# Performance work log

Measured on AMD Instinct MI355X. Metric: run time of the kernel, lower is better.

The kernel has to match this reference:

```python
import jax, jax.numpy as jnp
import numpy as np

B, P, ENC = 128, 196, 2048   # batch, num_pixels (14x14), encoder_dim
A, H, E, V = 512, 512, 512, 10000  # attention_dim, hidden, embed, vocab
T = 20  # max decode length (lengths max = T+1)


def setup_inputs() -> dict:
    key = jax.random.key(0)
    ks = jax.random.split(key, 24)
    def rn(k, shape, scale=0.05):
        return jax.random.normal(k, shape, jnp.float32) * scale
    encoder_out = jax.random.normal(ks[0], (B, P, ENC), jnp.float32)
    captions = jax.random.randint(ks[1], (B, T + 1), 0, V)
    # lengths sorted descending (packed-sequence convention), max forced to T+1
    lengths = jnp.sort(jax.random.randint(ks[2], (B,), 2, T + 2))[::-1]
    lengths = lengths.at[0].set(T + 1)
    return {
        "encoder_out": encoder_out,
        "captions": captions,
        "lengths": lengths,
        "W_enc_att": rn(ks[3], (A, ENC)), "b_enc_att": jnp.zeros((A,), jnp.float32),
        "W_dec_att": rn(ks[4], (A, H)),   "b_dec_att": jnp.zeros((A,), jnp.float32),
        "w_full_att": rn(ks[5], (1, A)),  "b_full_att": jnp.zeros((1,), jnp.float32),
        "emb_table": rn(ks[6], (V, E)),
        "W_ih": rn(ks[7], (4 * H, E + ENC)), "b_ih": jnp.zeros((4 * H,), jnp.float32),
        "W_hh": rn(ks[8], (4 * H, H)),       "b_hh": jnp.zeros((4 * H,), jnp.float32),
        "W_init_h": rn(ks[9], (H, ENC)),  "b_init_h": jnp.zeros((H,), jnp.float32),
        "W_init_c": rn(ks[10], (H, ENC)), "b_init_c": jnp.zeros((H,), jnp.float32),
        "W_fbeta": rn(ks[11], (ENC, H)),  "b_fbeta": jnp.zeros((ENC,), jnp.float32),
        "W_fc": rn(ks[12], (V, H)),       "b_fc": jnp.zeros((V,), jnp.float32),
    }


def reference(encoder_out, captions, lengths,
              W_enc_att, b_enc_att, W_dec_att, b_dec_att, w_full_att, b_full_att,
              emb_table, W_ih, b_ih, W_hh, b_hh,
              W_init_h, b_init_h, W_init_c, b_init_c,
              W_fbeta, b_fbeta, W_fc, b_fc):
    # Precompute encoder side of Bahdanau attention once (loop-invariant)
    att1 = jnp.einsum('bpe,ae->bpa', encoder_out, W_enc_att) + b_enc_att  # [B,P,A]
    emb = emb_table[captions]                                            # [B,T+1,E]
    mean_enc = encoder_out.mean(axis=1)                                  # [B,ENC]
    h0 = mean_enc @ W_init_h.T + b_init_h
    c0 = mean_enc @ W_init_c.T + b_init_c
    dec_len = lengths - 1
    # mask[t, b] = True while sample b still decodes at step t (== torch's b < batch_size_t for sorted lengths)
    mask = (jnp.arange(T)[:, None] < dec_len[None, :]).astype(encoder_out.dtype)  # [T,B]
    xs = (jnp.swapaxes(emb[:, :T, :], 0, 1), mask)  # ([T,B,E], [T,B])

    def step(carry, x):
        h, c = carry
        emb_t, m = x  # [B,E], [B]
        # Bahdanau attention
        att2 = h @ W_dec_att.T + b_dec_att                               # [B,A]
        e = jnp.einsum('bpa,a->bp', jax.nn.relu(att1 + att2[:, None, :]),
                       w_full_att[0]) + b_full_att[0]                    # [B,P]
        alpha = jax.nn.softmax(e, axis=1)
        context = jnp.einsum('bp,bpe->be', alpha, encoder_out)           # [B,ENC]
        gate = jax.nn.sigmoid(h @ W_fbeta.T + b_fbeta)
        context = gate * context
        # LSTMCell (PyTorch gate order: i, f, g, o); dropout is identity in eval mode
        x_in = jnp.concatenate([emb_t, context], axis=1)                 # [B,E+ENC]
        gates = x_in @ W_ih.T + b_ih + h @ W_hh.T + b_hh                 # [B,4H]
        i, f, g, o = jnp.split(gates, 4, axis=1)
        c_new = jax.nn.sigmoid(f) * c + jax.nn.sigmoid(i) * jnp.tanh(g)
        h_new = jax.nn.sigmoid(o) * jnp.tanh(c_new)
        pred = (h_new @ W_fc.T + b_fc) * m[:, None]                      # zeros past length
        mb = m[:, None]
        h = mb * h_new + (1.0 - mb) * h   # freeze state for finished rows
        c = mb * c_new + (1.0 - mb) * c
        return (h, c), pred

    (_, _), preds = jax.lax.scan(step, (h0, c0), xs)
    return jnp.swapaxes(preds, 0, 1)  # [B,T,V]
```

## Files before the change

### kernel.cpp

```cpp
#include <hip/hip_runtime.h>
#include <hip/hip_bf16.h>
#include <math.h>

#define B_   128
#define P_   196
#define ENC_ 2048
#define A_   512
#define H_   512
#define E_   512
#define V_   10000
#define T_   20
#define NDF_ 2560
#define XK_  3072
#define GK_  2560

typedef __attribute__((ext_vector_type(8))) short bf16x8;
typedef __attribute__((ext_vector_type(4))) short bf16x4;
typedef __attribute__((ext_vector_type(2))) short bf16x2;
typedef __attribute__((ext_vector_type(4))) float f32x4;

__device__ __forceinline__ float sigmoidf_(float x) { return 1.0f / (1.0f + expf(-x)); }

__device__ __forceinline__ short f2bf(float f) {
    unsigned u = __float_as_uint(f);
    u += 0x7fffu + ((u >> 16) & 1u);
    return (short)(u >> 16);
}
__device__ __forceinline__ float bf2f(short s) {
    return __uint_as_float(((unsigned)(unsigned short)s) << 16);
}
__device__ __forceinline__ void gload_lds16(const void* g, void* l) {
    __builtin_amdgcn_global_load_lds(
        (const __attribute__((address_space(1))) void*)g,
        (__attribute__((address_space(3))) void*)l, 16, 0, 0);
}

#define BM 128
#define BN 64
#define BK 64

#define COMPUTE64(ASP, BSP, CUR)                                               \
    _Pragma("unroll")                                                          \
    for (int kk = 0; kk < BK; kk += 32) {                                      \
        const int kb = (kk >> 3) + (lane >> 4);                                \
        bf16x8 av[4], bv[2];                                                   \
        _Pragma("unroll")                                                      \
        for (int i = 0; i < 4; i++) {                                          \
            int rr = wr * 64 + i * 16 + (lane & 15);                           \
            av[i] = *(const bf16x8*)&(ASP)[(CUR) * (BM * BK) + rr * BK         \
                    + ((kb ^ (rr & 7)) << 3)];                                 \
        }                                                                      \
        _Pragma("unroll")                                                      \
        for (int j = 0; j < 2; j++) {                                          \
            int cc = wc * 32 + j * 16 + (lane & 15);                           \
            bv[j] = *(const bf16x8*)&(BSP)[(CUR) * (BN * BK) + cc * BK         \
                    + ((kb ^ (cc & 7)) << 3)];                                 \
        }                                                                      \
        _Pragma("unroll")                                                      \
        for (int i = 0; i < 4; i++)                                            \
            _Pragma("unroll")                                                  \
            for (int j = 0; j < 2; j++)                                        \
                acc[i][j] = __builtin_amdgcn_mfma_f32_16x16x32_bf16(           \
                    av[i], bv[j], acc[i][j], 0, 0, 0);                         \
    }

__global__ __launch_bounds__(256) void gemm_bf(
    const short* __restrict__ A, const short* __restrict__ Bw,
    float* __restrict__ Cf, short* __restrict__ Cb,
    const float* __restrict__ bias,
    int N, int K, int lda, int ldb, int ldc,
    int mtiles, int ntiles, int mode,
    const int* __restrict__ lengths)
{
    __shared__ __attribute__((aligned(16))) short As[2][BM * BK];
    __shared__ __attribute__((aligned(16))) short Bs[2][BN * BK];
    int pm, pn;
    if (mtiles == 1) { pm = 0; pn = blockIdx.x; }
    else {
        int xcd = blockIdx.x & 7, s = blockIdx.x >> 3;
        pn = s % ntiles;
        pm = (s / ntiles) * 8 + xcd;
        if (pm >= mtiles) return;
    }
    const int bm = pm * BM, bn = pn * BN;
    const int tid = threadIdx.x, w = tid >> 6, lane = tid & 63;
    const int wr = w >> 1, wc = w & 1;
    const int lr8 = lane >> 3, lk = lane & 7;

    f32x4 zero4 = {0.f, 0.f, 0.f, 0.f};
    f32x4 acc[4][2];
    #pragma unroll
    for (int i = 0; i < 4; i++)
        #pragma unroll
        for (int j = 0; j < 2; j++) acc[i][j] = zero4;

#define STAGE(buf, k0) {                                                        \
    _Pragma("unroll")                                                           \
    for (int i = 0; i < 4; i++) {                                               \
        int row0 = w * 32 + i * 8; int row = row0 + lr8;                        \
        gload_lds16(A + (size_t)(bm + row) * lda + (k0)                         \
                    + ((lk ^ (row & 7)) << 3), &As[buf][row0 * BK]);            \
    }                                                                           \
    _Pragma("unroll")                                                           \
    for (int i = 0; i < 2; i++) {                                               \
        int row0 = w * 16 + i * 8; int row = row0 + lr8;                        \
        int gn = bn + row; if (gn > N - 1) gn = N - 1;                          \
        gload_lds16(Bw + (size_t)gn * ldb + (k0)                                \
                    + ((lk ^ (row & 7)) << 3), &Bs[buf][row0 * BK]);            \
    } }

    STAGE(0, 0);
    __syncthreads();
    int cur = 0;
    for (int k0 = 0; k0 < K; k0 += BK) {
        if (k0 + BK < K) STAGE(cur ^ 1, k0 + BK);
        COMPUTE64(&As[0][0], &Bs[0][0], cur);
        __syncthreads();
        cur ^= 1;
    }
#undef STAGE

    const int lr = lane >> 4, lc = lane & 15;
    #pragma unroll
    for (int i = 0; i < 4; i++) {
        #pragma unroll
        for (int r = 0; r < 4; r++) {
            int row = bm + wr * 64 + i * 16 + lr * 4 + r;
            #pragma unroll
            for (int j = 0; j < 2; j++) {
                int col = bn + wc * 32 + j * 16 + lc;
                if (col >= N) continue;
                float v = acc[i][j][r] + bias[col];
                if (mode == 1) {
                    int tt = row >> 7, bb = row & 127;
                    float rs = (tt < lengths[bb] - 1) ? 1.0f : 0.0f;
                    Cf[(size_t)bb * T_ * V_ + (size_t)tt * V_ + col] = v * rs;
                } else if (mode == 2) {
                    if (col < H_) Cb[(size_t)row * H_ + col] = f2bf(v);
                    else          Cf[(size_t)row * H_ + (col - H_)] = v;
                } else if (Cb) {
                    Cb[(size_t)row * ldc + col] = f2bf(v);
                } else {
                    Cf[(size_t)row * ldc + col] = v;
                }
            }
        }
    }
}

__global__ __launch_bounds__(256) void att1_gemm(
    const float* __restrict__ A, const short* __restrict__ Bw,
    short* __restrict__ Cb, const float* __restrict__ bias)
{
    __shared__ __attribute__((aligned(16))) short As[2][BM * BK];
    __shared__ __attribute__((aligned(16))) short Bs[2][BN * BK];
    int xcd = blockIdx.x & 7, s = blockIdx.x >> 3;
    int pn = s % 8;
    int pm = (s / 8) * 8 + xcd;
    if (pm >= 196) return;
    const int bm = pm * BM, bn = pn * BN;
    const int tid = threadIdx.x, w = tid >> 6, lane = tid & 63;
    const int wr = w >> 1, wc = w & 1;
    const int lr8 = lane >> 3, lk = lane & 7;

    f32x4 zero4 = {0.f, 0.f, 0.f, 0.f};
    f32x4 acc[4][2];
    #pragma unroll
    for (int i = 0; i < 4; i++)
        #pragma unroll
        for (int j = 0; j < 2; j++) acc[i][j] = zero4;

    float4 ra[4][2];
#define LOADA(k0) {                                                             \
    _Pragma("unroll")                                                           \
    for (int i = 0; i < 4; i++) {                                               \
        int row = w * 32 + i * 8 + lr8;                                         \
        const float* ga = A + (size_t)(bm + row) * ENC_ + (k0)                  \
                          + ((lk ^ (row & 7)) << 3);                            \
        ra[i][0] = *(const float4*)ga;                                          \
        ra[i][1] = *(const float4*)(ga + 4);                                    \
    } }
#define WRITEA(buf) {                                                           \
    _Pragma("unroll")                                                           \
    for (int i = 0; i < 4; i++) {                                               \
        int row = w * 32 + i * 8 + lr8;                                         \
        bf16x8 v;                                                               \
        v[0] = f2bf(ra[i][0].x); v[1] = f2bf(ra[i][0].y);                       \
        v[2] = f2bf(ra[i][0].z); v[3] = f2bf(ra[i][0].w);                       \
        v[4] = f2bf(ra[i][1].x); v[5] = f2bf(ra[i][1].y);                       \
        v[6] = f2bf(ra[i][1].z); v[7] = f2bf(ra[i][1].w);                       \
        *(bf16x8*)&As[buf][row * BK + (lk << 3)] = v;                           \
    } }
#define BSTAGE(buf, k0) {                                                       \
    _Pragma("unroll")                                                           \
    for (int i = 0; i < 2; i++) {                                               \
        int row0 = w * 16 + i * 8; int row = row0 + lr8;                        \
        gload_lds16(Bw + (size_t)(bn + row) * ENC_ + (k0)                       \
                    + ((lk ^ (row & 7)) << 3), &Bs[buf][row0 * BK]);            \
    } }

    LOADA(0);
    BSTAGE(0, 0);
    WRITEA(0);
    __syncthreads();
    int cur = 0;
    for (int k0 = 0; k0 < ENC_; k0 += BK) {
        if (k0 + BK < ENC_) { LOADA(k0 + BK); BSTAGE(cur ^ 1, k0 + BK); }
        COMPUTE64(&As[0][0], &Bs[0][0], cur);
        if (k0 + BK < ENC_) WRITEA(cur ^ 1);
        __syncthreads();
        cur ^= 1;
    }
#undef LOADA
#undef WRITEA
#undef BSTAGE

    const int lr = lane >> 4, lc = lane & 15;
    #pragma unroll
    for (int i = 0; i < 4; i++)
        #pragma unroll
        for (int r = 0; r < 4; r++) {
            int row = bm + wr * 64 + i * 16 + lr * 4 + r;
            #pragma unroll
            for (int j = 0; j < 2; j++) {
                int col = bn + wc * 32 + j * 16 + lc;
                Cb[(size_t)row * A_ + col] = f2bf(acc[i][j][r] + bias[col]);
            }
        }
}

__global__ __launch_bounds__(512) void esmctx_kernel(
    const short* __restrict__ att1_bf, const float* __restrict__ attf,
    const float* __restrict__ wfull, const short* __restrict__ enc_bf,
    short* __restrict__ ctxbuf, const int* __restrict__ lengths, int t)
{
    __shared__ float es[P_];
    __shared__ float red[256];
    __shared__ float al[P_];
    __shared__ float sm, ss;
    const int b = blockIdx.y, half = blockIdx.x;
    if (t >= lengths[b] - 1) return;
    const int tid = threadIdx.x, wv = tid >> 6, lane = tid & 63;

    float a2v[8], wv8[8];
    const float* a2 = attf + (size_t)b * NDF_;
    #pragma unroll
    for (int i = 0; i < 8; i++) {
        a2v[i] = a2[lane * 8 + i];
        wv8[i] = wfull[lane * 8 + i];
    }
    for (int row = wv; row < P_; row += 8) {
        bf16x8 a1 = *(const bf16x8*)(att1_bf + ((size_t)b * P_ + row) * A_ + lane * 8);
        float s = 0.0f;
        #pragma unroll
        for (int i = 0; i < 8; i++) {
            float v = bf2f(a1[i]) + a2v[i];
            s += fmaxf(v, 0.0f) * wv8[i];
        }
        #pragma unroll
        for (int off = 32; off > 0; off >>= 1) s += __shfl_down(s, off, 64);
        if (lane == 0) es[row] = s;
    }
    __syncthreads();
    float v = (tid < P_) ? es[tid] : -1e30f;
    if (tid < 256) red[tid] = v;
    __syncthreads();
    for (int rs = 128; rs > 0; rs >>= 1) {
        if (tid < rs) red[tid] = fmaxf(red[tid], red[tid + rs]);
        __syncthreads();
    }
    if (tid == 0) sm = red[0];
    __syncthreads();
    float ex = (tid < P_) ? expf(v - sm) : 0.0f;
    if (tid < 256) red[tid] = ex;
    __syncthreads();
    for (int rs = 128; rs > 0; rs >>= 1) {
        if (tid < rs) red[tid] += red[tid + rs];
        __syncthreads();
    }
    if (tid == 0) ss = red[0];
    __syncthreads();
    if (tid < P_) al[tid] = ex / ss;
    __syncthreads();

    const int c0 = half * 1024 + tid * 2;
    const short* eb = enc_bf + (size_t)b * P_ * ENC_ + c0;
    float s0 = 0, s1 = 0;
    for (int p = 0; p < P_; p++) {
        bf16x2 ev = *(const bf16x2*)(eb + (size_t)p * ENC_);
        float a = al[p];
        s0 += a * bf2f(ev[0]); s1 += a * bf2f(ev[1]);
    }
    const float* fb = attf + (size_t)b * NDF_ + A_;
    bf16x2 o;
    o[0] = f2bf(sigmoidf_(fb[c0 + 0]) * s0);
    o[1] = f2bf(sigmoidf_(fb[c0 + 1]) * s1);
    *(bf16x2*)(ctxbuf + (size_t)b * ENC_ + c0) = o;
}

__global__ __launch_bounds__(256) void gates_lstm(
    const short* __restrict__ ctxbuf, const short* __restrict__ hcur,
    short* __restrict__ hnxt,
    const short* __restrict__ Wcat, const float* __restrict__ gpre,
    float* __restrict__ cbuf, short* __restrict__ hn_t,
    const int* __restrict__ lengths, int t)
{
    __shared__ __attribute__((aligned(16))) char smem[49152];
    short* As0 = (short*)smem;
    short* Bs0 = (short*)(smem + 32768);
    const int bn = blockIdx.x * BN;
    const int tid = threadIdx.x, w = tid >> 6, lane = tid & 63;
    const int wr = w >> 1, wc = w & 1;
    const int lr8 = lane >> 3, lk = lane & 7;

    f32x4 zero4 = {0.f, 0.f, 0.f, 0.f};
    f32x4 acc[4][2];
    #pragma unroll
    for (int i = 0; i < 4; i++)
        #pragma unroll
        for (int j = 0; j < 2; j++) acc[i][j] = zero4;

#define STAGE_G(buf, k0) {                                                      \
    const short* Ap; int Al, kk0;                                               \
    if ((k0) < ENC_) { Ap = ctxbuf; Al = ENC_; kk0 = (k0); }                    \
    else             { Ap = hcur;   Al = H_;   kk0 = (k0) - ENC_; }             \
    _Pragma("unroll")                                                           \
    for (int i = 0; i < 4; i++) {                                               \
        int row0 = w * 32 + i * 8; int row = row0 + lr8;                        \
        gload_lds16(Ap + (size_t)row * Al + kk0 + ((lk ^ (row & 7)) << 3),      \
                    &As0[(buf) * (BM * BK) + row0 * BK]);                       \
    }                                                                           \
    _Pragma("unroll")                                                           \
    for (int i = 0; i < 2; i++) {                                               \
        int row0 = w * 16 + i * 8; int row = row0 + lr8;                        \
        gload_lds16(Wcat + (size_t)(bn + row) * XK_ + E_ + (k0)                 \
                    + ((lk ^ (row & 7)) << 3),                                  \
                    &Bs0[(buf) * (BN * BK) + row0 * BK]);                       \
    } }

    STAGE_G(0, 0);
    __syncthreads();
    int cur = 0;
    for (int k0 = 0; k0 < GK_; k0 += BK) {
        if (k0 + BK < GK_) STAGE_G(cur ^ 1, k0 + BK);
        COMPUTE64(As0, Bs0, cur);
        __syncthreads();
        cur ^= 1;
    }
#undef STAGE_G

    float* gl = (float*)smem;
    const int lr = lane >> 4, lc = lane & 15;
    #pragma unroll
    for (int i = 0; i < 4; i++)
        #pragma unroll
        for (int r = 0; r < 4; r++) {
            int row = wr * 64 + i * 16 + lr * 4 + r;
            #pragma unroll
            for (int j = 0; j < 2; j++) {
                int col = wc * 32 + j * 16 + lc;
                gl[row * 68 + col] = acc[i][j][r] + gpre[(size_t)row * (4 * H_) + bn + col];
            }
        }
    __syncthreads();
    #pragma unroll
    for (int q = 0; q < 8; q++) {
        int id  = tid * 8 + q;
        int row = id >> 4;
        int j   = id & 15;
        int jg  = (bn >> 2) + j;
        float i_ = sigmoidf_(gl[row * 68 + 4 * j + 0]);
        float f_ = sigmoidf_(gl[row * 68 + 4 * j + 1]);
        float g_ = tanhf    (gl[row * 68 + 4 * j + 2]);
        float o_ = sigmoidf_(gl[row * 68 + 4 * j + 3]);
        float cn = f_ * cbuf[row * H_ + jg] + i_ * g_;
        float hv = o_ * tanhf(cn);
        hn_t[row * H_ + jg] = f2bf(hv);
        bool m = t < lengths[row] - 1;
        if (m) cbuf[row * H_ + jg] = cn;
        hnxt[row * H_ + jg] = m ? f2bf(hv) : hcur[row * H_ + jg];
    }
}

__global__ __launch_bounds__(256) void castenc_mean(const float* __restrict__ enc,
                                                    short* __restrict__ enc_bf,
                                                    short* __restrict__ meanE_bf)
{
    const int b = blockIdx.y;
    const int c0 = blockIdx.x * 1024 + threadIdx.x * 4;
    const float* src = enc + (size_t)b * P_ * ENC_ + c0;
    short* dst = enc_bf + (size_t)b * P_ * ENC_ + c0;
    float s0 = 0, s1 = 0, s2 = 0, s3 = 0;
    for (int p = 0; p < P_; p++) {
        float4 f = *(const float4*)(src + (size_t)p * ENC_);
        bf16x4 v;
        v[0] = f2bf(f.x); v[1] = f2bf(f.y); v[2] = f2bf(f.z); v[3] = f2bf(f.w);
        *(bf16x4*)(dst + (size_t)p * ENC_) = v;
        s0 += f.x; s1 += f.y; s2 += f.z; s3 += f.w;
    }
    const float inv = 1.0f / (float)P_;
    bf16x4 m;
    m[0] = f2bf(s0 * inv); m[1] = f2bf(s1 * inv);
    m[2] = f2bf(s2 * inv); m[3] = f2bf(s3 * inv);
    *(bf16x4*)(meanE_bf + (size_t)b * ENC_ + c0) = m;
}

#define PB0 1024
#define PB1 (PB0 + 2048)
#define PB2 (PB1 + 5000)
#define PB3 (PB2 + 1280)
#define PB4 (PB3 + 6144)
#define PB5 (PB4 + 1280)
#define PB6 (PB5 + 3)
#define PB7 (PB6 + 2)
#define PB8 (PB7 + 1)

__device__ __forceinline__ void cast4(const float* __restrict__ in,
                                      short* __restrict__ out, int i4) {
    float4 f = *(const float4*)(in + i4);
    bf16x4 v;
    v[0] = f2bf(f.x); v[1] = f2bf(f.y); v[2] = f2bf(f.z); v[3] = f2bf(f.w);
    *(bf16x4*)(out + i4) = v;
}
__device__ __forceinline__ void cast4p(const float* __restrict__ src,
                                       short* __restrict__ out, int i4) {
    float4 f = *(const float4*)src;
    bf16x4 v;
    v[0] = f2bf(f.x); v[1] = f2bf(f.y); v[2] = f2bf(f.z); v[3] = f2bf(f.w);
    *(bf16x4*)(out + i4) = v;
}

__global__ __launch_bounds__(256) void prep_kernel(
    const float* __restrict__ W_enc,    const float* __restrict__ W_init_h,
    const float* __restrict__ W_init_c, const float* __restrict__ W_fc,
    const float* __restrict__ W_dec,    const float* __restrict__ W_fbeta,
    const float* __restrict__ W_ih,     const float* __restrict__ W_hh,
    const int*   __restrict__ captions, const float* __restrict__ emb_tab,
    const float* __restrict__ b_dec,    const float* __restrict__ b_fbeta,
    const float* __restrict__ b_ih,     const float* __restrict__ b_hh,
    const float* __restrict__ b_init_h, const float* __restrict__ b_init_c,
    short* __restrict__ Wenc_bf,  short* __restrict__ Winit_bf,
    short* __restrict__ Wfc_bf,   short* __restrict__ Wdf_bf,
    short* __restrict__ Wcat_bf,  short* __restrict__ emb_all,
    float* __restrict__ bdf,      float* __restrict__ bcat,
    float* __restrict__ binit)
{
    const int blk = blockIdx.x, tid = threadIdx.x;
    if (blk < PB0) {
        cast4(W_enc, Wenc_bf, blk * 1024 + tid * 4);
    } else if (blk < PB1) {
        int i4 = (blk - PB0) * 1024 + tid * 4;
        int n = i4 >> 11, k = i4 & 2047;
        const float* src = (n < H_) ? W_init_h + (size_t)n * ENC_ + k
                                    : W_init_c + (size_t)(n - H_) * ENC_ + k;
        cast4p(src, Winit_bf, i4);
    } else if (blk < PB2) {
        cast4(W_fc, Wfc_bf, (blk - PB1) * 1024 + tid * 4);
    } else if (blk < PB3) {
        int i4 = (blk - PB2) * 1024 + tid * 4;
        int n = i4 >> 9, k = i4 & 511;
        const float* src = (n < A_) ? W_dec + (size_t)n * H_ + k
                                    : W_fbeta + (size_t)(n - A_) * H_ + k;
        cast4p(src, Wdf_bf, i4);
    } else if (blk < PB4) {
        int i4 = (blk - PB3) * 1024 + tid * 4;
        int n = i4 / XK_, k = i4 - n * XK_;
        int srow = (n & 3) * H_ + (n >> 2);
        const float* src = (k < E_ + ENC_) ? W_ih + (size_t)srow * (E_ + ENC_) + k
                                           : W_hh + (size_t)srow * H_ + (k - (E_ + ENC_));
        cast4p(src, Wcat_bf, i4);
    } else if (blk < PB5) {
        int i4 = (blk - PB4) * 1024 + tid * 4;
        int col = i4 & 511;
        int bt  = i4 >> 9;
        int b   = bt & 127;
        int tt  = bt >> 7;
        int tok = captions[b * (T_ + 1) + tt];
        cast4p(emb_tab + (size_t)tok * E_ + col, emb_all, i4);
    } else if (blk < PB6) {
        int j = (blk - PB5) * 1024 + tid * 4;
        #pragma unroll
        for (int q = 0; q < 4; q++, j++)
            if (j < NDF_) bdf[j] = (j < A_) ? b_dec[j] : b_fbeta[j - A_];
    } else if (blk < PB7) {
        int j = (blk - PB6) * 1024 + tid * 4;
        #pragma unroll
        for (int q = 0; q < 4; q++, j++) {
            int srow = (j & 3) * H_ + (j >> 2);
            bcat[j] = b_ih[srow] + b_hh[srow];
        }
    } else {
        int j = tid * 4;
        #pragma unroll
        for (int q = 0; q < 4; q++, j++)
            binit[j] = (j < H_) ? b_init_h[j] : b_init_c[j - H_];
    }
}

extern "C" void kernel_launch(void* const* d_in, const int* in_sizes, int n_in,
                              void* d_out, int out_size, void* d_ws, size_t ws_size,
                              hipStream_t stream)
{
    const float* enc      = (const float*)d_in[0];
    const int*   captions = (const int*)  d_in[1];
    const int*   lengths  = (const int*)  d_in[2];
    const float* W_enc    = (const float*)d_in[3];
    const float* b_enc    = (const float*)d_in[4];
    const float* W_dec    = (const float*)d_in[5];
    const float* b_dec    = (const float*)d_in[6];
    const float* w_full   = (const float*)d_in[7];
    const float* emb_tab  = (const float*)d_in[9];
    const float* W_ih     = (const float*)d_in[10];
    const float* b_ih     = (const float*)d_in[11];
    const float* W_hh     = (const float*)d_in[12];
    const float* b_hh     = (const float*)d_in[13];
    const float* W_init_h = (const float*)d_in[14];
    const float* b_init_h = (const float*)d_in[15];
    const float* W_init_c = (const float*)d_in[16];
    const float* b_init_c = (const float*)d_in[17];
    const float* W_fbeta  = (const float*)d_in[18];
    const float* b_fbeta  = (const float*)d_in[19];
    const float* W_fc     = (const float*)d_in[20];
    const float* b_fc     = (const float*)d_in[21];
    float* out = (float*)d_out;

    char* ws = (char*)d_ws;
    size_t off = 0;
    auto alloc = [&](size_t bytes) { void* p = ws + off; off += (bytes + 255) & ~(size_t)255; return p; };
    short* enc_bf    = (short*)alloc((size_t)B_ * P_ * ENC_ * 2);
    short* att1_bf   = (short*)alloc((size_t)B_ * P_ * A_ * 2);
    short* Wenc_bf   = (short*)alloc((size_t)A_ * ENC_ * 2);
    short* Winit_bf  = (short*)alloc((size_t)2 * H_ * ENC_ * 2);
    short* Wdf_bf    = (short*)alloc((size_t)NDF_ * H_ * 2);
    short* Wcat_bf   = (short*)alloc((size_t)4 * H_ * XK_ * 2);
    short* Wfc_bf    = (short*)alloc((size_t)V_ * H_ * 2);
    float* bdf       = (float*)alloc(NDF_ * 4);
    float* bcat      = (float*)alloc(4 * H_ * 4);
    float* binit     = (float*)alloc(2 * H_ * 4);
    short* meanE_bf  = (short*)alloc((size_t)B_ * ENC_ * 2);
    float* cbuf      = (float*)alloc((size_t)B_ * H_ * 4);
    short* hbufs     = (short*)alloc((size_t)2 * B_ * H_ * 2);
    short* emb_all   = (short*)alloc((size_t)T_ * B_ * E_ * 2);
    short* hn_all    = (short*)alloc((size_t)T_ * B_ * H_ * 2);
    float* attf      = (float*)alloc((size_t)B_ * NDF_ * 4);
    short* ctxbuf    = (short*)alloc((size_t)B_ * ENC_ * 2);
    float* gates_pre = (float*)alloc((size_t)T_ * B_ * 4 * H_ * 4);
    (void)ws_size;

    prep_kernel<<<PB8, 256, 0, stream>>>(
        W_enc, W_init_h, W_init_c, W_fc, W_dec, W_fbeta, W_ih, W_hh,
        captions, emb_tab, b_dec, b_fbeta, b_ih, b_hh, b_init_h, b_init_c,
        Wenc_bf, Winit_bf, Wfc_bf, Wdf_bf, Wcat_bf, emb_all, bdf, bcat, binit);

    att1_gemm<<<8 * 8 * ((196 + 7) / 8), 256, 0, stream>>>(
        enc, Wenc_bf, att1_bf, b_enc);
    castenc_mean<<<dim3(2, B_), 256, 0, stream>>>(enc, enc_bf, meanE_bf);
    gemm_bf<<<8 * 32 * (((T_ * B_) / BM + 7) / 8), 256, 0, stream>>>(
        emb_all, Wcat_bf, gates_pre, nullptr, bcat,
        4 * H_, E_, E_, XK_, 4 * H_, (T_ * B_) / BM, 32, 0, nullptr);
    gemm_bf<<<(2 * H_) / BN, 256, 0, stream>>>(
        meanE_bf, Winit_bf, cbuf, hbufs, binit,
        2 * H_, ENC_, ENC_, ENC_, 0, 1, (2 * H_) / BN, 2, nullptr);

    for (int t = 0; t < T_; t++) {
        short* hcur = hbufs + (size_t)(t & 1) * B_ * H_;
        short* hnxt = hbufs + (size_t)((t & 1) ^ 1) * B_ * H_;
        gemm_bf<<<NDF_ / BN, 256, 0, stream>>>(
            hcur, Wdf_bf, attf, nullptr, bdf,
            NDF_, H_, H_, H_, NDF_, 1, NDF_ / BN, 0, nullptr);
        esmctx_kernel<<<dim3(2, B_), 512, 0, stream>>>(
            att1_bf, attf, w_full, enc_bf, ctxbuf, lengths, t);
        gates_lstm<<<(4 * H_) / BN, 256, 0, stream>>>(
            ctxbuf, hcur, hnxt, Wcat_bf, gates_pre + (size_t)t * B_ * 4 * H_,
            cbuf, hn_all + (size_t)t * B_ * H_, lengths, t);
    }
    gemm_bf<<<8 * 157 * (((T_ * B_) / BM + 7) / 8), 256, 0, stream>>>(
        hn_all, Wfc_bf, out, nullptr, b_fc,
        V_, H_, H_, H_, 0, (T_ * B_) / BM, 157, 1, lengths);
}
```

Baseline: 1.883 ms.

## Fuse decode loop into persistent cooperative kernel with grid barriers

The 20-step decode loop, previously three kernel launches per step (attention projection GEMM, energy/softmax/context, gates+LSTM), becomes a single cooperative persistent kernel of 256 blocks that synchronise through an atomic-counter grid barrier between phases. This is meant to remove about 60 launch gaps and their tail effects. The att1 GEMM also now reads the already bf16-cast encoder through the generic gemm_bf path, dropping the dedicated fp32-input kernel. The cost is three spin barriers per step and idle blocks in the GEMM phases; if the cooperative launch fails, the old launch loop runs instead.

```diff
diff --git a/kernel.cpp b/kernel.cpp
--- a/kernel.cpp
+++ b/kernel.cpp
@@ -13,6 +13,7 @@
 #define NDF_ 2560
 #define XK_  3072
 #define GK_  2560
+#define NBLK_ 256
 
 typedef __attribute__((ext_vector_type(8))) short bf16x8;
 typedef __attribute__((ext_vector_type(4))) short bf16x4;
@@ -148,85 +149,238 @@
     }
 }
 
-__global__ __launch_bounds__(256) void att1_gemm(
-    const float* __restrict__ A, const short* __restrict__ Bw,
-    short* __restrict__ Cb, const float* __restrict__ bias)
+__device__ __forceinline__ void gbar(unsigned* cnt, unsigned target) {
+    __syncthreads();
+    if (threadIdx.x == 0) {
+        __hip_atomic_fetch_add(cnt, 1u, __ATOMIC_RELEASE, __HIP_MEMORY_SCOPE_AGENT);
+        while (__hip_atomic_fetch_add(cnt, 0u, __ATOMIC_RELAXED, __HIP_MEMORY_SCOPE_AGENT) < target)
+            __builtin_amdgcn_s_sleep(8);
+        (void)__hip_atomic_load(cnt, __ATOMIC_ACQUIRE, __HIP_MEMORY_SCOPE_AGENT);
+    }
+    __syncthreads();
+}
+
+__global__ __launch_bounds__(512) void loop_kernel(
+    const short* __restrict__ att1_bf, const short* __restrict__ enc_bf,
+    const short* __restrict__ Wdf, const float* __restrict__ bdf,
+    const float* __restrict__ wfull, const short* __restrict__ Wcat,
+    const float* __restrict__ gates_pre,
+    short* __restrict__ hbufs, float* __restrict__ cbuf,
+    short* __restrict__ hn_all, float* __restrict__ attf,
+    short* __restrict__ ctxbuf, const int* __restrict__ lengths,
+    unsigned* __restrict__ cnt)
 {
-    __shared__ __attribute__((aligned(16))) short As[2][BM * BK];
-    __shared__ __attribute__((aligned(16))) short Bs[2][BN * BK];
-    int xcd = blockIdx.x & 7, s = blockIdx.x >> 3;
-    int pn = s % 8;
-    int pm = (s / 8) * 8 + xcd;
-    if (pm >= 196) return;
-    const int bm = pm * BM, bn = pn * BN;
-    const int tid = threadIdx.x, w = tid >> 6, lane = tid & 63;
-    const int wr = w >> 1, wc = w & 1;
+    __shared__ __attribute__((aligned(16))) char smem[49152];
+    const int blk = blockIdx.x, tid = threadIdx.x;
+    const int lane = tid & 63;
+    const bool act = tid < 256;
+    const int w4 = (tid >> 6) & 3;
+    const int wr = w4 >> 1, wc = w4 & 1;
     const int lr8 = lane >> 3, lk = lane & 7;
-
-    f32x4 zero4 = {0.f, 0.f, 0.f, 0.f};
-    f32x4 acc[4][2];
-    #pragma unroll
-    for (int i = 0; i < 4; i++)
-        #pragma unroll
-        for (int j = 0; j < 2; j++) acc[i][j] = zero4;
-
-    float4 ra[4][2];
-#define LOADA(k0) {                                                             \
+    const int lr = lane >> 4, lc = lane & 15;
+    unsigned bar = 0;
+
+#define STAGE_A(buf, k0) if (act) {                                             \
     _Pragma("unroll")                                                           \
     for (int i = 0; i < 4; i++) {                                               \
-        int row = w * 32 + i * 8 + lr8;                                         \
-        const float* ga = A + (size_t)(bm + row) * ENC_ + (k0)                  \
-                          + ((lk ^ (row & 7)) << 3);                            \
-        ra[i][0] = *(const float4*)ga;                                          \
-        ra[i][1] = *(const float4*)(ga + 4);                                    \
+        int row0 = w4 * 32 + i * 8; int row = row0 + lr8;                       \
+        gload_lds16(hcur + (size_t)row * H_ + (k0) + ((lk ^ (row & 7)) << 3),   \
+                    &As0[(buf) * (BM * BK) + row0 * BK]);                       \
+    }                                                                           \
+    _Pragma("unroll")                                                           \
+    for (int i = 0; i < 2; i++) {                                               \
+        int row0 = w4 * 16 + i * 8; int row = row0 + lr8;                       \
+        gload_lds16(Wdf + (size_t)(bn + row) * H_ + (k0)                        \
+                    + ((lk ^ (row & 7)) << 3),                                  \
+                    &Bs0[(buf) * (BN * BK) + row0 * BK]);                       \
     } }
-#define WRITEA(buf) {                                                           \
+
+#define STAGE_C(buf, k0) if (act) {                                             \
+    const short* Ap; int Al, kk0;                                               \
+    if ((k0) < ENC_) { Ap = ctxbuf; Al = ENC_; kk0 = (k0); }                    \
+    else             { Ap = hcur;   Al = H_;   kk0 = (k0) - ENC_; }             \
     _Pragma("unroll")                                                           \
     for (int i = 0; i < 4; i++) {                                               \
-        int row = w * 32 + i * 8 + lr8;                                         \
-        bf16x8 v;                                                               \
-        v[0] = f2bf(ra[i][0].x); v[1] = f2bf(ra[i][0].y);                       \
-        v[2] = f2bf(ra[i][0].z); v[3] = f2bf(ra[i][0].w);                       \
-        v[4] = f2bf(ra[i][1].x); v[5] = f2bf(ra[i][1].y);                       \
-        v[6] = f2bf(ra[i][1].z); v[7] = f2bf(ra[i][1].w);                       \
-        *(bf16x8*)&As[buf][row * BK + (lk << 3)] = v;                           \
-    } }
-#define BSTAGE(buf, k0) {                                                       \
+        int row0 = w4 * 32 + i * 8; int row = row0 + lr8;                       \
+        gload_lds16(Ap + (size_t)row * Al + kk0 + ((lk ^ (row & 7)) << 3),      \
+                    &As0[(buf) * (BM * BK) + row0 * BK]);                       \
+    }                                                                           \
     _Pragma("unroll")                                                           \
     for (int i = 0; i < 2; i++) {                                               \
-        int row0 = w * 16 + i * 8; int row = row0 + lr8;                        \
-        gload_lds16(Bw + (size_t)(bn + row) * ENC_ + (k0)                       \
-                    + ((lk ^ (row & 7)) << 3), &Bs[buf][row0 * BK]);            \
+        int row0 = w4 * 16 + i * 8; int row = row0 + lr8;                       \
+        gload_lds16(Wcat + (size_t)(bn + row) * XK_ + E_ + (k0)                 \
+                    + ((lk ^ (row & 7)) << 3),                                  \
+                    &Bs0[(buf) * (BN * BK) + row0 * BK]);                       \
     } }
 
-    LOADA(0);
-    BSTAGE(0, 0);
-    WRITEA(0);
-    __syncthreads();
-    int cur = 0;
-    for (int k0 = 0; k0 < ENC_; k0 += BK) {
-        if (k0 + BK < ENC_) { LOADA(k0 + BK); BSTAGE(cur ^ 1, k0 + BK); }
-        COMPUTE64(&As[0][0], &Bs[0][0], cur);
-        if (k0 + BK < ENC_) WRITEA(cur ^ 1);
-        __syncthreads();
-        cur ^= 1;
-    }
-#undef LOADA
-#undef WRITEA
-#undef BSTAGE
-
-    const int lr = lane >> 4, lc = lane & 15;
-    #pragma unroll
-    for (int i = 0; i < 4; i++)
-        #pragma unroll
-        for (int r = 0; r < 4; r++) {
-            int row = bm + wr * 64 + i * 16 + lr * 4 + r;
-            #pragma unroll
-            for (int j = 0; j < 2; j++) {
-                int col = bn + wc * 32 + j * 16 + lc;
-                Cb[(size_t)row * A_ + col] = f2bf(acc[i][j][r] + bias[col]);
+    for (int t = 0; t < T_; t++) {
+        const short* hcur = hbufs + (size_t)(t & 1) * B_ * H_;
+        short* hnxt = hbufs + (size_t)((t & 1) ^ 1) * B_ * H_;
+
+        if (blk < NDF_ / BN) {
+            short* As0 = (short*)smem;
+            short* Bs0 = (short*)(smem + 32768);
+            const int bn = blk * BN;
+            f32x4 acc[4][2];
+            if (act) {
+                f32x4 z = {0.f, 0.f, 0.f, 0.f};
+                #pragma unroll
+                for (int i = 0; i < 4; i++)
+                    #pragma unroll
+                    for (int j = 0; j < 2; j++) acc[i][j] = z;
+            }
+            STAGE_A(0, 0);
+            __syncthreads();
+            int cur = 0;
+            for (int k0 = 0; k0 < H_; k0 += BK) {
+                if (k0 + BK < H_) STAGE_A(cur ^ 1, k0 + BK);
+                if (act) { COMPUTE64(As0, Bs0, cur); }
+                __syncthreads();
+                cur ^= 1;
+            }
+            if (act) {
+                #pragma unroll
+                for (int i = 0; i < 4; i++)
+                    #pragma unroll
+                    for (int r = 0; r < 4; r++) {
+                        int row = wr * 64 + i * 16 + lr * 4 + r;
+                        #pragma unroll
+                        for (int j = 0; j < 2; j++) {
+                            int col = bn + wc * 32 + j * 16 + lc;
+                            attf[(size_t)row * NDF_ + col] = acc[i][j][r] + bdf[col];
+                        }
+                    }
             }
         }
+        bar++; gbar(cnt, bar * NBLK_);
+
+        {
+            const int b = blk >> 1, half = blk & 1;
+            if (t < lengths[b] - 1) {
+                float* es  = (float*)smem;
+                float* red = es + 256;
+                float* al  = red + 256;
+                float* st  = al + 256;
+                float a2v[8], wv8[8];
+                const float* a2 = attf + (size_t)b * NDF_;
+                #pragma unroll
+                for (int i = 0; i < 8; i++) {
+                    a2v[i] = a2[lane * 8 + i];
+                    wv8[i] = wfull[lane * 8 + i];
+                }
+                for (int row = tid >> 6; row < P_; row += 8) {
+                    bf16x8 a1 = *(const bf16x8*)(att1_bf + ((size_t)b * P_ + row) * A_ + lane * 8);
+                    float s = 0.0f;
+                    #pragma unroll
+                    for (int i = 0; i < 8; i++) {
+                        float v = bf2f(a1[i]) + a2v[i];
+                        s += fmaxf(v, 0.0f) * wv8[i];
+                    }
+                    #pragma unroll
+                    for (int off = 32; off > 0; off >>= 1) s += __shfl_down(s, off, 64);
+                    if (lane == 0) es[row] = s;
+                }
+                __syncthreads();
+                float v = (tid < P_) ? es[tid] : -1e30f;
+                if (tid < 256) red[tid] = v;
+                __syncthreads();
+                for (int rs = 128; rs > 0; rs >>= 1) {
+                    if (tid < rs) red[tid] = fmaxf(red[tid], red[tid + rs]);
+                    __syncthreads();
+                }
+                if (tid == 0) st[0] = red[0];
+                __syncthreads();
+                float ex = (tid < P_) ? expf(v - st[0]) : 0.0f;
+                if (tid < 256) red[tid] = ex;
+                __syncthreads();
+                for (int rs = 128; rs > 0; rs >>= 1) {
+                    if (tid < rs) red[tid] += red[tid + rs];
+                    __syncthreads();
+                }
+                if (tid == 0) st[1] = red[0];
+                __syncthreads();
+                if (tid < P_) al[tid] = ex / st[1];
+                __syncthreads();
+
+                const int c0 = half * 1024 + tid * 2;
+                const short* eb = enc_bf + (size_t)b * P_ * ENC_ + c0;
+                float s0 = 0, s1 = 0;
+                for (int p = 0; p < P_; p++) {
+                    bf16x2 ev = *(const bf16x2*)(eb + (size_t)p * ENC_);
+                    float a = al[p];
+                    s0 += a * bf2f(ev[0]); s1 += a * bf2f(ev[1]);
+                }
+                const float* fb = attf + (size_t)b * NDF_ + A_;
+                bf16x2 o;
+                o[0] = f2bf(sigmoidf_(fb[c0 + 0]) * s0);
+                o[1] = f2bf(sigmoidf_(fb[c0 + 1]) * s1);
+                *(bf16x2*)(ctxbuf + (size_t)b * ENC_ + c0) = o;
+            }
+        }
+        bar++; gbar(cnt, bar * NBLK_);
+
+        if (blk < (4 * H_) / BN) {
+            short* As0 = (short*)smem;
+            short* Bs0 = (short*)(smem + 32768);
+            short* hn_t = hn_all + (size_t)t * B_ * H_;
+            const int bn = blk * BN;
+            const float* gpre = gates_pre + (size_t)t * B_ * 4 * H_;
+            f32x4 acc[4][2];
+            if (act) {
+                f32x4 z = {0.f, 0.f, 0.f, 0.f};
+                #pragma unroll
+                for (int i = 0; i < 4; i++)
+                    #pragma unroll
+                    for (int j = 0; j < 2; j++) acc[i][j] = z;
+            }
+            STAGE_C(0, 0);
+            __syncthreads();
+            int cur = 0;
+            for (int k0 = 0; k0 < GK_; k0 += BK) {
+                if (k0 + BK < GK_) STAGE_C(cur ^ 1, k0 + BK);
+                if (act) { COMPUTE64(As0, Bs0, cur); }
+                __syncthreads();
+                cur ^= 1;
+            }
+            float* gl = (float*)smem;
+            if (act) {
+                #pragma unroll
+                for (int i = 0; i < 4; i++)
+                    #pragma unroll
+                    for (int r = 0; r < 4; r++) {
+                        int row = wr * 64 + i * 16 + lr * 4 + r;
+                        #pragma unroll
+                        for (int j = 0; j < 2; j++) {
+                            int col = wc * 32 + j * 16 + lc;
+                            gl[row * 68 + col] = acc[i][j][r] + gpre[(size_t)row * (4 * H_) + bn + col];
+                        }
+                    }
+            }
+            __syncthreads();
+            if (act) {
+                #pragma unroll
+                for (int q = 0; q < 8; q++) {
+                    int id  = tid * 8 + q;
+                    int row = id >> 4;
+                    int j   = id & 15;
+                    int jg  = (bn >> 2) + j;
+                    float i_ = sigmoidf_(gl[row * 68 + 4 * j + 0]);
+                    float f_ = sigmoidf_(gl[row * 68 + 4 * j + 1]);
+                    float g_ = tanhf    (gl[row * 68 + 4 * j + 2]);
+                    float o_ = sigmoidf_(gl[row * 68 + 4 * j + 3]);
+                    float cn = f_ * cbuf[row * H_ + jg] + i_ * g_;
+                    float hv = o_ * tanhf(cn);
+                    hn_t[row * H_ + jg] = f2bf(hv);
+                    bool m = t < lengths[row] - 1;
+                    if (m) cbuf[row * H_ + jg] = cn;
+                    hnxt[row * H_ + jg] = m ? f2bf(hv) : hcur[row * H_ + jg];
+                }
+            }
+        }
+        bar++; gbar(cnt, bar * NBLK_);
+    }
+#undef STAGE_A
+#undef STAGE_C
 }
 
 __global__ __launch_bounds__(512) void esmctx_kernel(
@@ -443,7 +597,7 @@
     short* __restrict__ Wfc_bf,   short* __restrict__ Wdf_bf,
     short* __restrict__ Wcat_bf,  short* __restrict__ emb_all,
     float* __restrict__ bdf,      float* __restrict__ bcat,
-    float* __restrict__ binit)
+    float* __restrict__ binit,    unsigned* __restrict__ cnt)
 {
     const int blk = blockIdx.x, tid = threadIdx.x;
     if (blk < PB0) {
@@ -494,6 +648,8 @@
         #pragma unroll
         for (int q = 0; q < 4; q++, j++)
             binit[j] = (j < H_) ? b_init_h[j] : b_init_c[j - H_];
+        if (tid == 0)
+            __hip_atomic_store(cnt, 0u, __ATOMIC_RELEASE, __HIP_MEMORY_SCOPE_AGENT);
     }
 }
 
@@ -545,16 +701,17 @@
     float* attf      = (float*)alloc((size_t)B_ * NDF_ * 4);
     short* ctxbuf    = (short*)alloc((size_t)B_ * ENC_ * 2);
     float* gates_pre = (float*)alloc((size_t)T_ * B_ * 4 * H_ * 4);
+    unsigned* cnt    = (unsigned*)alloc(256);
     (void)ws_size;
 
     prep_kernel<<<PB8, 256, 0, stream>>>(
         W_enc, W_init_h, W_init_c, W_fc, W_dec, W_fbeta, W_ih, W_hh,
         captions, emb_tab, b_dec, b_fbeta, b_ih, b_hh, b_init_h, b_init_c,
-        Wenc_bf, Winit_bf, Wfc_bf, Wdf_bf, Wcat_bf, emb_all, bdf, bcat, binit);
-
-    att1_gemm<<<8 * 8 * ((196 + 7) / 8), 256, 0, stream>>>(
-        enc, Wenc_bf, att1_bf, b_enc);
+        Wenc_bf, Winit_bf, Wfc_bf, Wdf_bf, Wcat_bf, emb_all, bdf, bcat, binit, cnt);
     castenc_mean<<<dim3(2, B_), 256, 0, stream>>>(enc, enc_bf, meanE_bf);
+    gemm_bf<<<8 * 8 * ((196 + 7) / 8), 256, 0, stream>>>(
+        enc_bf, Wenc_bf, nullptr, att1_bf, b_enc,
+        A_, ENC_, ENC_, ENC_, A_, 196, 8, 0, nullptr);
     gemm_bf<<<8 * 32 * (((T_ * B_) / BM + 7) / 8), 256, 0, stream>>>(
         emb_all, Wcat_bf, gates_pre, nullptr, bcat,
         4 * H_, E_, E_, XK_, 4 * H_, (T_ * B_) / BM, 32, 0, nullptr);
@@ -562,18 +719,31 @@
         meanE_bf, Winit_bf, cbuf, hbufs, binit,
         2 * H_, ENC_, ENC_, ENC_, 0, 1, (2 * H_) / BN, 2, nullptr);
 
-    for (int t = 0; t < T_; t++) {
-        short* hcur = hbufs + (size_t)(t & 1) * B_ * H_;
-        short* hnxt = hbufs + (size_t)((t & 1) ^ 1) * B_ * H_;
-        gemm_bf<<<NDF_ / BN, 256, 0, stream>>>(
-            hcur, Wdf_bf, attf, nullptr, bdf,
-            NDF_, H_, H_, H_, NDF_, 1, NDF_ / BN, 0, nullptr);
-        esmctx_kernel<<<dim3(2, B_), 512, 0, stream>>>(
-            att1_bf, attf, w_full, enc_bf, ctxbuf, lengths, t);
-        gates_lstm<<<(4 * H_) / BN, 256, 0, stream>>>(
-            ctxbuf, hcur, hnxt, Wcat_bf, gates_pre + (size_t)t * B_ * 4 * H_,
-            cbuf, hn_all + (size_t)t * B_ * H_, lengths, t);
-    }
+    {
+        void* kargs[] = {
+            (void*)&att1_bf, (void*)&enc_bf, (void*)&Wdf_bf, (void*)&bdf,
+            (void*)&w_full, (void*)&Wcat_bf, (void*)&gates_pre,
+            (void*)&hbufs, (void*)&cbuf, (void*)&hn_all, (void*)&attf,
+            (void*)&ctxbuf, (void*)&lengths, (void*)&cnt
+        };
+        hipError_t cerr = hipLaunchCooperativeKernel(
+            (const void*)loop_kernel, dim3(NBLK_), dim3(512), kargs, 0, stream);
+        if (cerr != hipSuccess) {
+            for (int t = 0; t < T_; t++) {
+                short* hcur = hbufs + (size_t)(t & 1) * B_ * H_;
+                short* hnxt = hbufs + (size_t)((t & 1) ^ 1) * B_ * H_;
+                gemm_bf<<<NDF_ / BN, 256, 0, stream>>>(
+                    hcur, Wdf_bf, attf, nullptr, bdf,
+                    NDF_, H_, H_, H_, NDF_, 1, NDF_ / BN, 0, nullptr);
+                esmctx_kernel<<<dim3(2, B_), 512, 0, stream>>>(
+                    att1_bf, attf, w_full, enc_bf, ctxbuf, lengths, t);
+                gates_lstm<<<(4 * H_) / BN, 256, 0, stream>>>(
+                    ctxbuf, hcur, hnxt, Wcat_bf, gates_pre + (size_t)t * B_ * 4 * H_,
+                    cbuf, hn_all + (size_t)t * B_ * H_, lengths, t);
+            }
+        }
+    }
+
     gemm_bf<<<8 * 157 * (((T_ * B_) / BM + 7) / 8), 256, 0, stream>>>(
         hn_all, Wfc_bf, out, nullptr, b_fc,
         V_, H_, H_, H_, 0, (T_ * B_) / BM, 157, 1, lengths);
```

Measured after the change: 3.393 ms. +80.2%, slower.

## Feed att1 GEMM from pre-cast bf16 encoder with 64-row tiles

Applied to the files above, without the earlier changes.

The att1 projection no longer reads fp32 encoder_out and converts it to bf16 in registers. It now runs after castenc_mean and reads the bf16 encoder copy through direct global-to-LDS loads, using a generic 64-row-tile bf16 GEMM, which doubles the number of M tiles. castenc_mean also switches to nontemporal loads for the fp32 encoder stream. The aim is to halve the A-side bytes the GEMM reads and drop the register staging and conversion. The cost is that the GEMM now depends on the cast kernel finishing, and the smaller tiles reload the B weights more often.

```diff
diff --git a/kernel.cpp b/kernel.cpp
--- a/kernel.cpp
+++ b/kernel.cpp
@@ -148,83 +148,86 @@
     }
 }
 
-__global__ __launch_bounds__(256) void att1_gemm(
-    const float* __restrict__ A, const short* __restrict__ Bw,
-    short* __restrict__ Cb, const float* __restrict__ bias)
-{
-    __shared__ __attribute__((aligned(16))) short As[2][BM * BK];
+__global__ __launch_bounds__(256) void gemm_bf64(
+    const short* __restrict__ A, const short* __restrict__ Bw,
+    short* __restrict__ Cb, const float* __restrict__ bias,
+    int N, int K, int lda, int ldb, int ldc,
+    int mtiles, int ntiles)
+{
+    __shared__ __attribute__((aligned(16))) short As[2][64 * BK];
     __shared__ __attribute__((aligned(16))) short Bs[2][BN * BK];
     int xcd = blockIdx.x & 7, s = blockIdx.x >> 3;
-    int pn = s % 8;
-    int pm = (s / 8) * 8 + xcd;
-    if (pm >= 196) return;
-    const int bm = pm * BM, bn = pn * BN;
+    int pn = s % ntiles;
+    int pm = (s / ntiles) * 8 + xcd;
+    if (pm >= mtiles) return;
+    const int bm = pm * 64, bn = pn * BN;
     const int tid = threadIdx.x, w = tid >> 6, lane = tid & 63;
     const int wr = w >> 1, wc = w & 1;
     const int lr8 = lane >> 3, lk = lane & 7;
 
     f32x4 zero4 = {0.f, 0.f, 0.f, 0.f};
-    f32x4 acc[4][2];
-    #pragma unroll
-    for (int i = 0; i < 4; i++)
+    f32x4 acc[2][2];
+    #pragma unroll
+    for (int i = 0; i < 2; i++)
         #pragma unroll
         for (int j = 0; j < 2; j++) acc[i][j] = zero4;
 
-    float4 ra[4][2];
-#define LOADA(k0) {                                                             \
-    _Pragma("unroll")                                                           \
-    for (int i = 0; i < 4; i++) {                                               \
-        int row = w * 32 + i * 8 + lr8;                                         \
-        const float* ga = A + (size_t)(bm + row) * ENC_ + (k0)                  \
-                          + ((lk ^ (row & 7)) << 3);                            \
-        ra[i][0] = *(const float4*)ga;                                          \
-        ra[i][1] = *(const float4*)(ga + 4);                                    \
-    } }
-#define WRITEA(buf) {                                                           \
-    _Pragma("unroll")                                                           \
-    for (int i = 0; i < 4; i++) {                                               \
-        int row = w * 32 + i * 8 + lr8;                                         \
-        bf16x8 v;                                                               \
-        v[0] = f2bf(ra[i][0].x); v[1] = f2bf(ra[i][0].y);                       \
-        v[2] = f2bf(ra[i][0].z); v[3] = f2bf(ra[i][0].w);                       \
-        v[4] = f2bf(ra[i][1].x); v[5] = f2bf(ra[i][1].y);                       \
-        v[6] = f2bf(ra[i][1].z); v[7] = f2bf(ra[i][1].w);                       \
-        *(bf16x8*)&As[buf][row * BK + (lk << 3)] = v;                           \
-    } }
-#define BSTAGE(buf, k0) {                                                       \
+#define STAGE64(buf, k0) {                                                      \
     _Pragma("unroll")                                                           \
     for (int i = 0; i < 2; i++) {                                               \
         int row0 = w * 16 + i * 8; int row = row0 + lr8;                        \
-        gload_lds16(Bw + (size_t)(bn + row) * ENC_ + (k0)                       \
+        gload_lds16(A + (size_t)(bm + row) * lda + (k0)                         \
+                    + ((lk ^ (row & 7)) << 3), &As[buf][row0 * BK]);            \
+    }                                                                           \
+    _Pragma("unroll")                                                           \
+    for (int i = 0; i < 2; i++) {                                               \
+        int row0 = w * 16 + i * 8; int row = row0 + lr8;                        \
+        int gn = bn + row; if (gn > N - 1) gn = N - 1;                          \
+        gload_lds16(Bw + (size_t)gn * ldb + (k0)                                \
                     + ((lk ^ (row & 7)) << 3), &Bs[buf][row0 * BK]);            \
     } }
 
-    LOADA(0);
-    BSTAGE(0, 0);
-    WRITEA(0);
+    STAGE64(0, 0);
     __syncthreads();
     int cur = 0;
-    for (int k0 = 0; k0 < ENC_; k0 += BK) {
-        if (k0 + BK < ENC_) { LOADA(k0 + BK); BSTAGE(cur ^ 1, k0 + BK); }
-        COMPUTE64(&As[0][0], &Bs[0][0], cur);
-        if (k0 + BK < ENC_) WRITEA(cur ^ 1);
+    for (int k0 = 0; k0 < K; k0 += BK) {
+        if (k0 + BK < K) STAGE64(cur ^ 1, k0 + BK);
+        #pragma unroll
+        for (int kk = 0; kk < BK; kk += 32) {
+            const int kb = (kk >> 3) + (lane >> 4);
+            bf16x8 av[2], bv[2];
+            #pragma unroll
+            for (int i = 0; i < 2; i++) {
+                int rr = wr * 32 + i * 16 + (lane & 15);
+                av[i] = *(const bf16x8*)&As[cur][rr * BK + ((kb ^ (rr & 7)) << 3)];
+            }
+            #pragma unroll
+            for (int j = 0; j < 2; j++) {
+                int cc = wc * 32 + j * 16 + (lane & 15);
+                bv[j] = *(const bf16x8*)&Bs[cur][cc * BK + ((kb ^ (cc & 7)) << 3)];
+            }
+            #pragma unroll
+            for (int i = 0; i < 2; i++)
+                #pragma unroll
+                for (int j = 0; j < 2; j++)
+                    acc[i][j] = __builtin_amdgcn_mfma_f32_16x16x32_bf16(
+                        av[i], bv[j], acc[i][j], 0, 0, 0);
+        }
         __syncthreads();
         cur ^= 1;
     }
-#undef LOADA
-#undef WRITEA
-#undef BSTAGE
+#undef STAGE64
 
     const int lr = lane >> 4, lc = lane & 15;
     #pragma unroll
-    for (int i = 0; i < 4; i++)
+    for (int i = 0; i < 2; i++)
         #pragma unroll
         for (int r = 0; r < 4; r++) {
-            int row = bm + wr * 64 + i * 16 + lr * 4 + r;
+            int row = bm + wr * 32 + i * 16 + lr * 4 + r;
             #pragma unroll
             for (int j = 0; j < 2; j++) {
                 int col = bn + wc * 32 + j * 16 + lc;
-                Cb[(size_t)row * A_ + col] = f2bf(acc[i][j][r] + bias[col]);
+                if (col < N) Cb[(size_t)row * ldc + col] = f2bf(acc[i][j][r] + bias[col]);
             }
         }
 }
@@ -388,15 +391,15 @@
 {
     const int b = blockIdx.y;
     const int c0 = blockIdx.x * 1024 + threadIdx.x * 4;
-    const float* src = enc + (size_t)b * P_ * ENC_ + c0;
+    const f32x4* src = (const f32x4*)(enc + (size_t)b * P_ * ENC_ + c0);
     short* dst = enc_bf + (size_t)b * P_ * ENC_ + c0;
     float s0 = 0, s1 = 0, s2 = 0, s3 = 0;
     for (int p = 0; p < P_; p++) {
-        float4 f = *(const float4*)(src + (size_t)p * ENC_);
+        f32x4 f = __builtin_nontemporal_load(src + (size_t)p * (ENC_ / 4));
         bf16x4 v;
-        v[0] = f2bf(f.x); v[1] = f2bf(f.y); v[2] = f2bf(f.z); v[3] = f2bf(f.w);
+        v[0] = f2bf(f[0]); v[1] = f2bf(f[1]); v[2] = f2bf(f[2]); v[3] = f2bf(f[3]);
         *(bf16x4*)(dst + (size_t)p * ENC_) = v;
-        s0 += f.x; s1 += f.y; s2 += f.z; s3 += f.w;
+        s0 += f[0]; s1 += f[1]; s2 += f[2]; s3 += f[3];
     }
     const float inv = 1.0f / (float)P_;
     bf16x4 m;
@@ -551,10 +554,10 @@
         W_enc, W_init_h, W_init_c, W_fc, W_dec, W_fbeta, W_ih, W_hh,
         captions, emb_tab, b_dec, b_fbeta, b_ih, b_hh, b_init_h, b_init_c,
         Wenc_bf, Winit_bf, Wfc_bf, Wdf_bf, Wcat_bf, emb_all, bdf, bcat, binit);
-
-    att1_gemm<<<8 * 8 * ((196 + 7) / 8), 256, 0, stream>>>(
-        enc, Wenc_bf, att1_bf, b_enc);
     castenc_mean<<<dim3(2, B_), 256, 0, stream>>>(enc, enc_bf, meanE_bf);
+    gemm_bf64<<<8 * 8 * ((392 + 7) / 8), 256, 0, stream>>>(
+        enc_bf, Wenc_bf, att1_bf, b_enc,
+        A_, ENC_, ENC_, ENC_, A_, 392, 8);
     gemm_bf<<<8 * 32 * (((T_ * B_) / BM + 7) / 8), 256, 0, stream>>>(
         emb_all, Wcat_bf, gates_pre, nullptr, bcat,
         4 * H_, E_, E_, XK_, 4 * H_, (T_ * B_) / BM, 32, 0, nullptr);
```

After: 1.820 ms. 1.03x faster.
